# Performance work log

Hardware: AMD Instinct MI355X
Metric: run time of the kernel (lower is better)

## Reference

```python
import jax, jax.numpy as jnp
import numpy as np
from jax import lax

B, N, D, E, P, K, H = 32, 512, 512, 8, 96, 25, 4
PAD = 12  # conv padding so length is preserved


def setup_inputs() -> dict:
    key = jax.random.key(0)
    ks = jax.random.split(key, 16)
    s = 0.05  # weight scale to keep softmax/cosine well-conditioned
    x = jax.random.normal(ks[0], (B, N, D), dtype=jnp.float32)
    router = jax.random.normal(ks[1], (1, E, D), dtype=jnp.float32)
    Wq = jax.random.normal(ks[2], (D, D), dtype=jnp.float32) * s
    bq = jax.random.normal(ks[3], (D,), dtype=jnp.float32) * s
    Wk = jax.random.normal(ks[4], (D, D), dtype=jnp.float32) * s
    bk = jax.random.normal(ks[5], (D,), dtype=jnp.float32) * s
    Wv = jax.random.normal(ks[6], (D, D), dtype=jnp.float32) * s
    bv = jax.random.normal(ks[7], (D,), dtype=jnp.float32) * s
    Wo = jax.random.normal(ks[8], (D, D), dtype=jnp.float32) * s
    bo = jax.random.normal(ks[9], (D,), dtype=jnp.float32) * s
    Wc = jax.random.normal(ks[10], (E, 2, K), dtype=jnp.float32) * s  # E experts' Conv1d(2,1,25) stacked as out-channels
    bc = jax.random.normal(ks[11], (E,), dtype=jnp.float32) * s
    Wp = jax.random.normal(ks[12], (E, D, P), dtype=jnp.float32) * s  # E experts' Linear(D,P), stored (in,out)
    bp = jax.random.normal(ks[13], (E, P), dtype=jnp.float32) * s
    return {"x": x, "router": router, "Wq": Wq, "bq": bq, "Wk": Wk, "bk": bk,
            "Wv": Wv, "bv": bv, "Wo": Wo, "bo": bo, "Wc": Wc, "bc": bc,
            "Wp": Wp, "bp": bp}


def _forward(x, router, Wq, bq, Wk, bk, Wv, bv, Wo, bo, Wc, bc, Wp, bp):
    b, n, d = x.shape
    e = router.shape[1]
    dk = d // H
    r = jnp.broadcast_to(router, (b, e, d))
    # multi-head attention: queries=router slots, keys/values=x (dropout = identity at eval)
    q = (r @ Wq + bq).reshape(b, e, H, dk)
    k = (x @ Wk + bk).reshape(b, n, H, dk)
    v = (x @ Wv + bv).reshape(b, n, H, dk)
    scale = 1.0 / jnp.sqrt(jnp.asarray(dk, x.dtype))
    scores = jnp.einsum('blhe,bshe->bhls', q, k)  # [b,H,e,n]
    A = jax.nn.softmax(scale * scores, axis=-1)
    att = jnp.einsum('bhls,bshd->blhd', A, v).reshape(b, e, d)
    att = att @ Wo + bo  # [b,e,d]
    # cosine-similarity routing score, mapped to (1+pi)/2
    dot = jnp.einsum('bed,bnd->ben', att, x)
    norm_a = jnp.linalg.norm(att, axis=2, keepdims=True)          # [b,e,1]
    norm_x = jnp.linalg.norm(x, axis=2)[:, None, :]                # [b,1,n]
    score = (1.0 + dot / (norm_a * norm_x)) / 2.0                  # [b,e,n]
    idx = jnp.argmax(score, axis=1)                                # [b,n] expert per token
    z = jnp.take_along_axis(att, idx[:, :, None], axis=1)          # [b,n,d]
    result = jnp.stack([x, z], axis=-2).reshape(b * n, 2, d)       # [bn,2,d]
    # run all E expert convs at once (experts stacked as output channels)
    conv_out = lax.conv_general_dilated(
        result, Wc, window_strides=(1,), padding=[(PAD, PAD)],
        dimension_numbers=('NCH', 'OIH', 'NCH')) + bc[None, :, None]  # [bn,E,d]
    lin = jnp.einsum('nel,elp->nep', conv_out, Wp) + bp[None]         # [bn,E,P]
    flat_idx = idx.reshape(-1)
    out = jnp.take_along_axis(lin, flat_idx[:, None, None], axis=1)[:, 0, :]
    return out.reshape(b, n, P)


def reference(x, router, Wq, bq, Wk, bk, Wv, bv, Wo, bo, Wc, bc, Wp, bp):
    return _forward(x, router, Wq, bq, Wk, bk, Wv, bv, Wo, bo, Wc, bc, Wp, bp)
```

## Files before the change

kernel.cpp:

```cpp
#include <hip/hip_runtime.h>
#include <hip/hip_bf16.h>

#define B_ 32
#define N_ 512
#define D_ 512
#define E_ 8
#define P_ 96
#define KC 25
#define H_ 4
#define DK 128
#define HE 32
#define BN 16384

typedef short short8 __attribute__((ext_vector_type(8)));
typedef float f32x4 __attribute__((ext_vector_type(4)));

#define OCNT  4096
#define OS2   4352
#define OM    5120
#define OC    21504
#define OA    21536
#define OATT  676896
#define OTOK  807968
#define OWEFF 939040
#define OZC   1332256
#define OUP   1356832

__device__ __forceinline__ float b2f(short s) {
  unsigned u = ((unsigned)(unsigned short)s) << 16;
  return __builtin_bit_cast(float, u);
}
__device__ __forceinline__ unsigned short f2b(float f) {
  return __builtin_bit_cast(unsigned short, __float2bfloat16(f));
}

__global__ __launch_bounds__(256) void k_head(const float* __restrict__ router,
        const float* __restrict__ Wq, const float* __restrict__ bq,
        const float* __restrict__ Wk, const float* __restrict__ bk,
        const float* __restrict__ Wp, const float* __restrict__ Wc,
        float* __restrict__ M, float* __restrict__ c,
        int* __restrict__ cnt, float* __restrict__ s2,
        __hip_bfloat16* __restrict__ weff) {
  __shared__ float sm[5824];
  int bid = blockIdx.x;
  int tid = threadIdx.x;
  if (bid < 64) {
    float* rs = sm;
    float* ps = sm + 512;
    float* qs = sm + 768;
    int he = bid >> 1, ch = bid & 1;
    int h = he >> 3, e = he & 7;
    for (int i = tid; i < 512; i += 256) rs[i] = router[e * D_ + i];
    __syncthreads();
    {
      int j = tid & 127, dh = tid >> 7;
      const float* wq = Wq + h * 128 + j;
      float acc = 0.f;
      for (int d = dh * 256; d < dh * 256 + 256; d += 4) {
        acc = fmaf(rs[d], wq[d * D_], acc);
        acc = fmaf(rs[d + 1], wq[(d + 1) * D_], acc);
        acc = fmaf(rs[d + 2], wq[(d + 2) * D_], acc);
        acc = fmaf(rs[d + 3], wq[(d + 3) * D_], acc);
      }
      ps[dh * 128 + j] = acc;
    }
    __syncthreads();
    if (tid < 128) qs[tid] = ps[tid] + ps[128 + tid] + bq[h * 128 + tid];
    __syncthreads();
    {
      int d0 = ch * 256 + tid;
      const float* wrow = Wk + d0 * D_ + h * 128;
      float acc = 0.f;
      for (int jj = 0; jj < 128; jj += 4) {
        float4 wv = *(const float4*)(wrow + jj);
        acc = fmaf(wv.x, qs[jj], acc);
        acc = fmaf(wv.y, qs[jj + 1], acc);
        acc = fmaf(wv.z, qs[jj + 2], acc);
        acc = fmaf(wv.w, qs[jj + 3], acc);
      }
      M[he * D_ + d0] = acc;
    }
    if (ch == 0 && tid < 64) {
      float s = qs[tid] * bk[h * 128 + tid] + qs[tid + 64] * bk[h * 128 + tid + 64];
#pragma unroll
      for (int off = 32; off; off >>= 1) s += __shfl_xor(s, off);
      if (tid == 0) c[he] = s;
    }
  } else if (bid < 192) {
    float* T = sm;
    float* wcs = sm + 5760;
    int eb = bid - 64;
    int e = eb >> 4, mc = eb & 15;
    int lo = mc * 32 - 12;
    for (int idx = tid; idx < 56 * 24; idx += 256) {
      int lp = idx / 24, p4 = (idx - lp * 24) * 4;
      int l = lo + lp;
      float4 v = {0.f, 0.f, 0.f, 0.f};
      if (l >= 0 && l < D_) v = *(const float4*)(Wp + (e * D_ + l) * P_ + p4);
      T[p4 * 60 + lp] = v.x; T[(p4 + 1) * 60 + lp] = v.y;
      T[(p4 + 2) * 60 + lp] = v.z; T[(p4 + 3) * 60 + lp] = v.w;
    }
    if (tid < 50) wcs[tid] = Wc[e * 2 * KC + tid];
    __syncthreads();
    int m = tid & 31, pg = tid >> 5;
#pragma unroll
    for (int j = 0; j < 2; ++j)
      for (int k2 = 0; k2 < 12; ++k2) {
        int p = pg * 12 + k2;
        float acc = 0.f;
#pragma unroll
        for (int k = 0; k < KC; ++k)
          acc = fmaf(wcs[j * 25 + k], T[p * 60 + m - k + 24], acc);
        weff[(((e * 2 + j) * P_ + p) << 9) + mc * 32 + m] = __float2bfloat16(acc);
      }
  } else {
    int e = bid - 192;
    if (bid == 192) cnt[tid] = 0;
    if (tid < 192) {
      int p = tid % 96, lg = tid / 96;
      float s = 0.f;
      const float* wp = Wp + e * D_ * P_ + p;
      for (int l = lg * 256; l < lg * 256 + 256; ++l) s += wp[l * P_];
      sm[lg * 96 + p] = s;
    }
    __syncthreads();
    if (tid < 96) s2[e * 96 + tid] = sm[tid] + sm[96 + tid];
  }
}

__global__ __launch_bounds__(128) void k_logits(const float* __restrict__ x,
        const float* __restrict__ M, float* __restrict__ A0,
        float* __restrict__ A1) {
  __shared__ float xs[64 * 132];
  __shared__ float Ms[32 * 132];
  int dh = blockIdx.x & 1;
  int nt8 = (blockIdx.x >> 1) & 7;
  int b = blockIdx.x >> 4;
  int tid = threadIdx.x;
  const float* xb = x + (b * N_ + nt8 * 64) * D_ + dh * 256;
  const float* Mb = M + dh * 256;
  float acc[4][4] = {{0.f}};
  for (int kc = 0; kc < 2; ++kc) {
    for (int idx = tid; idx < 2048; idx += 128) {
      int r = idx >> 5, c4 = (idx & 31) * 4;
      *(float4*)(xs + r * 132 + c4) = *(const float4*)(xb + r * D_ + kc * 128 + c4);
    }
    for (int idx = tid; idx < 1024; idx += 128) {
      int r = idx >> 5, c4 = (idx & 31) * 4;
      *(float4*)(Ms + r * 132 + c4) = *(const float4*)(Mb + r * D_ + kc * 128 + c4);
    }
    __syncthreads();
    int nt = tid & 15, ht = tid >> 4;
#pragma unroll 4
    for (int d4 = 0; d4 < 128; d4 += 4) {
      float4 xv[4], mv[4];
#pragma unroll
      for (int i = 0; i < 4; ++i)
        xv[i] = *(const float4*)(xs + (nt + 16 * i) * 132 + d4);
#pragma unroll
      for (int j = 0; j < 4; ++j)
        mv[j] = *(const float4*)(Ms + (ht + 8 * j) * 132 + d4);
#pragma unroll
      for (int i = 0; i < 4; ++i)
#pragma unroll
        for (int j = 0; j < 4; ++j) {
          float s = acc[i][j];
          s = fmaf(xv[i].x, mv[j].x, s);
          s = fmaf(xv[i].y, mv[j].y, s);
          s = fmaf(xv[i].z, mv[j].z, s);
          s = fmaf(xv[i].w, mv[j].w, s);
          acc[i][j] = s;
        }
    }
    __syncthreads();
  }
  int nt = tid & 15, ht = tid >> 4;
  float* Ad = dh ? A1 : A0;
#pragma unroll
  for (int j = 0; j < 4; ++j) {
    int he = ht + 8 * j;
#pragma unroll
    for (int i = 0; i < 4; ++i)
      Ad[(b * HE + he) * N_ + nt8 * 64 + nt + 16 * i] = acc[i][j];
  }
}

__global__ __launch_bounds__(256) void k_softmax(float* __restrict__ A0,
        const float* __restrict__ A1, const float* __restrict__ c) {
  int row = blockIdx.x;
  float* p0 = A0 + row * N_;
  const float* p1 = A1 + row * N_;
  float cc = c[row & 31];
  int t = threadIdx.x;
  const float scale = 0.08838834764831845f;
  float v0 = scale * (p0[t] + p1[t] + cc);
  float v1 = scale * (p0[t + 256] + p1[t + 256] + cc);
  __shared__ float red[4], red2[4];
  float m = fmaxf(v0, v1);
#pragma unroll
  for (int off = 32; off; off >>= 1) m = fmaxf(m, __shfl_xor(m, off));
  if ((t & 63) == 0) red[t >> 6] = m;
  __syncthreads();
  m = fmaxf(fmaxf(red[0], red[1]), fmaxf(red[2], red[3]));
  float e0 = expf(v0 - m), e1 = expf(v1 - m);
  float s = e0 + e1;
#pragma unroll
  for (int off = 32; off; off >>= 1) s += __shfl_xor(s, off);
  if ((t & 63) == 0) red2[t >> 6] = s;
  __syncthreads();
  s = red2[0] + red2[1] + red2[2] + red2[3];
  float inv = 1.0f / s;
  p0[t] = e0 * inv;
  p0[t + 256] = e1 * inv;
}

__global__ __launch_bounds__(512) void k_u2(const float* __restrict__ x,
        const float* __restrict__ A, float* __restrict__ up) {
  __shared__ float As[64 * 33];
  int nq = blockIdx.x, b = blockIdx.y;
  for (int idx = threadIdx.x; idx < 64 * 32; idx += 512) {
    int n = idx & 63, he = idx >> 6;
    As[n * 33 + he] = A[(b * HE + he) * N_ + nq * 64 + n];
  }
  __syncthreads();
  int dq = threadIdx.x & 127, hg = threadIdx.x >> 7;
  const float* xb = x + (b * N_ + nq * 64) * D_ + dq * 4;
  float acc[8][4];
#pragma unroll
  for (int j = 0; j < 8; ++j)
#pragma unroll
    for (int k = 0; k < 4; ++k) acc[j][k] = 0.f;
  for (int n = 0; n < 64; ++n) {
    float4 xv = *(const float4*)(xb + n * D_);
    const float* ar = As + n * 33 + hg * 8;
#pragma unroll
    for (int j = 0; j < 8; ++j) {
      float a = ar[j];
      acc[j][0] = fmaf(a, xv.x, acc[j][0]);
      acc[j][1] = fmaf(a, xv.y, acc[j][1]);
      acc[j][2] = fmaf(a, xv.z, acc[j][2]);
      acc[j][3] = fmaf(a, xv.w, acc[j][3]);
    }
  }
  float* o = up + (((b * 8 + nq) * HE) + hg * 8) * D_ + dq * 4;
#pragma unroll
  for (int j = 0; j < 8; ++j) {
    float4 v; v.x = acc[j][0]; v.y = acc[j][1]; v.z = acc[j][2]; v.w = acc[j][3];
    *(float4*)(o + j * D_) = v;
  }
}

__global__ __launch_bounds__(512) void k_vo3(const float* __restrict__ up,
        const float* __restrict__ Wv, const float* __restrict__ bv,
        const float* __restrict__ Wo, const float* __restrict__ bo,
        float* __restrict__ att) {
  __shared__ float us[4 * 512];
  __shared__ float part[4 * 512];
  __shared__ float ap_s[512];
  int b = blockIdx.x >> 3, e = blockIdx.x & 7;
  int tid = threadIdx.x;
  for (int idx = tid; idx < 4 * 128; idx += 512) {
    int h = idx >> 7, d4 = (idx & 127) * 4;
    const float* base = up + ((b * 8) * HE + h * 8 + e) * D_ + d4;
    float4 s = {0.f, 0.f, 0.f, 0.f};
#pragma unroll
    for (int nq = 0; nq < 8; ++nq) {
      float4 v = *(const float4*)(base + nq * HE * D_);
      s.x += v.x; s.y += v.y; s.z += v.z; s.w += v.w;
    }
    *(float4*)(us + h * 512 + d4) = s;
  }
  __syncthreads();
  {
    int cch = tid >> 7, j = tid & 127;
    int i0 = j * 4;
    int h = j >> 5;
    const float* ur = us + h * 512;
    const float* wv = Wv + i0;
    float4 acc = {0.f, 0.f, 0.f, 0.f};
    int d0 = cch * 128;
#pragma unroll 4
    for (int d = d0; d < d0 + 128; ++d) {
      float4 wq = *(const float4*)(wv + d * D_);
      float a = ur[d];
      acc.x = fmaf(a, wq.x, acc.x);
      acc.y = fmaf(a, wq.y, acc.y);
      acc.z = fmaf(a, wq.z, acc.z);
      acc.w = fmaf(a, wq.w, acc.w);
    }
    *(float4*)(part + cch * 512 + i0) = acc;
  }
  __syncthreads();
  ap_s[tid] = part[tid] + part[512 + tid] + part[1024 + tid] + part[1536 + tid]
              + bv[tid];
  __syncthreads();
  {
    int cch = tid >> 7, j = tid & 127;
    int o0 = j * 4;
    const float* wo = Wo + o0;
    float4 acc = {0.f, 0.f, 0.f, 0.f};
    int i0 = cch * 128;
#pragma unroll 4
    for (int i = i0; i < i0 + 128; ++i) {
      float4 wq = *(const float4*)(wo + i * D_);
      float a = ap_s[i];
      acc.x = fmaf(a, wq.x, acc.x);
      acc.y = fmaf(a, wq.y, acc.y);
      acc.z = fmaf(a, wq.z, acc.z);
      acc.w = fmaf(a, wq.w, acc.w);
    }
    *(float4*)(part + cch * 512 + o0) = acc;
  }
  __syncthreads();
  att[(b * E_ + e) * D_ + tid] = part[tid] + part[512 + tid] + part[1024 + tid]
                                 + part[1536 + tid] + bo[tid];
}

__global__ __launch_bounds__(256) void k_route2(const float* __restrict__ x,
        const float* __restrict__ att, const __hip_bfloat16* __restrict__ weff,
        const float* __restrict__ s2, const float* __restrict__ bc,
        const float* __restrict__ bp, int* __restrict__ cnt,
        int* __restrict__ tok, float* __restrict__ zc) {
  __shared__ float att_s[8 * D_];
  __shared__ float rn[8];
  __shared__ float red[4][520];
  __shared__ int blist[8][32];
  __shared__ int bcnt[8];
  int b = blockIdx.x >> 4, tile = blockIdx.x & 15;
  for (int idx = threadIdx.x; idx < 1024; idx += 256)
    *(float4*)(att_s + idx * 4) = *(const float4*)(att + b * E_ * D_ + idx * 4);
  if (threadIdx.x < 8) bcnt[threadIdx.x] = 0;
  __syncthreads();
  {
    int e = threadIdx.x >> 5, l = threadIdx.x & 31;
    float s = 0.f;
    for (int d0 = l; d0 < D_; d0 += 32) {
      float v = att_s[e * D_ + d0];
      s = fmaf(v, v, s);
    }
#pragma unroll
    for (int off = 16; off; off >>= 1) s += __shfl_xor(s, off);
    if (l == 0) rn[e] = 1.0f / sqrtf(s);
  }
  __syncthreads();
  int w = threadIdx.x >> 6, lane = threadIdx.x & 63;
  int e2 = lane & 7, ch = lane >> 3;
  float* rw = red[w];
  for (int i = 0; i < 8; ++i) {
    int t = b * N_ + tile * 32 + w * 8 + i;
    const float* xp = x + t * D_ + lane * 8;
    float4 xa = *(const float4*)xp;
    float4 xb4 = *(const float4*)(xp + 4);
    float p[8];
#pragma unroll
    for (int e = 0; e < 8; ++e) {
      const float* apt = att_s + e * D_ + lane * 8;
      float4 a0 = *(const float4*)apt;
      float4 a1 = *(const float4*)(apt + 4);
      float s = a0.x * xa.x;
      s = fmaf(a0.y, xa.y, s); s = fmaf(a0.z, xa.z, s); s = fmaf(a0.w, xa.w, s);
      s = fmaf(a1.x, xb4.x, s); s = fmaf(a1.y, xb4.y, s);
      s = fmaf(a1.z, xb4.z, s); s = fmaf(a1.w, xb4.w, s);
      p[e] = s;
    }
#pragma unroll
    for (int e = 0; e < 8; ++e) rw[e * 65 + lane] = p[e];
    float s = 0.f;
#pragma unroll
    for (int k = 0; k < 8; ++k) s += rw[e2 * 65 + ch * 8 + k];
    s += __shfl_xor(s, 8); s += __shfl_xor(s, 16); s += __shfl_xor(s, 32);
    float sc = s * rn[e2];
    int be = e2;
#pragma unroll
    for (int off = 1; off < 8; off <<= 1) {
      float o = __shfl_xor(sc, off);
      int oe = __shfl_xor(be, off);
      if (o > sc || (o == sc && oe < be)) { sc = o; be = oe; }
    }
    if (lane == 0) {
      int slot = atomicAdd(&bcnt[be], 1);
      blist[be][slot] = t;
    }
  }
  __syncthreads();
  {
    int e = threadIdx.x >> 5, r = threadIdx.x & 31;
    int ce = bcnt[e];
    int gs = 0;
    if (r == 0 && ce > 0) gs = atomicAdd(&cnt[e * 32], ce);
    gs = __shfl(gs, (threadIdx.x & 63) & 32);
    for (int k2 = r; k2 < ce; k2 += 32) tok[e * BN + gs + k2] = blist[e][k2];
  }
  int grp = threadIdx.x >> 4, l16 = threadIdx.x & 15;
  for (int r = 0; r < 3; ++r) {
    int P = tile * 48 + r * 16 + grp;
    int ez = P / 96, p = P - ez * 96;
    const short* wrow = (const short*)weff + (((ez * 2 + 1) * P_ + p) << 9);
    const float* arow = att_s + ez * D_;
    float acc = 0.f;
#pragma unroll
    for (int seg = 0; seg < 4; ++seg) {
      int d = seg * 128 + l16 * 8;
      short8 w8 = *(const short8*)(wrow + d);
      const float* a8 = arow + d;
      acc = fmaf(a8[0], b2f(w8[0]), acc); acc = fmaf(a8[1], b2f(w8[1]), acc);
      acc = fmaf(a8[2], b2f(w8[2]), acc); acc = fmaf(a8[3], b2f(w8[3]), acc);
      acc = fmaf(a8[4], b2f(w8[4]), acc); acc = fmaf(a8[5], b2f(w8[5]), acc);
      acc = fmaf(a8[6], b2f(w8[6]), acc); acc = fmaf(a8[7], b2f(w8[7]), acc);
    }
    acc += __shfl_xor(acc, 1); acc += __shfl_xor(acc, 2);
    acc += __shfl_xor(acc, 4); acc += __shfl_xor(acc, 8);
    if (l16 == 0)
      zc[(b * E_ + ez) * P_ + p] = acc + bc[ez] * s2[ez * 96 + p] + bp[ez * 96 + p];
  }
}

__global__ __launch_bounds__(256) void k_final(const float* __restrict__ x,
        const __hip_bfloat16* __restrict__ weff, const float* __restrict__ zc,
        const int* __restrict__ cnt, const int* __restrict__ tok,
        float* __restrict__ out) {
  __shared__ __align__(16) unsigned short xsb[32 * 520];
  __shared__ int toks[32];
  int g = blockIdx.x;
  int cl_e[E_], bs[E_ + 1];
  bs[0] = 0;
#pragma unroll
  for (int e = 0; e < E_; ++e) {
    cl_e[e] = cnt[e * 32];
    bs[e + 1] = bs[e] + ((cl_e[e] + 31) >> 5);
  }
  if (g >= bs[E_]) return;
  int e = 0;
#pragma unroll
  for (int k = 1; k < E_; ++k) if (g >= bs[k]) e = k;
  int base = (g - bs[e]) * 32;
  int cnt_e = cl_e[e];
  int cl = cnt_e - base; if (cl > 32) cl = 32;
  int tid = threadIdx.x;
  if (tid < 32) toks[tid] = (tid < cl) ? tok[e * BN + base + tid] : tok[e * BN + base];
  __syncthreads();
  for (int idx = tid; idx < 32 * 128; idx += 256) {
    int r = idx >> 7, c4 = (idx & 127) * 4;
    float4 v = *(const float4*)(x + toks[r] * D_ + c4);
    ushort4 u4;
    u4.x = f2b(v.x); u4.y = f2b(v.y); u4.z = f2b(v.z); u4.w = f2b(v.w);
    *(ushort4*)(xsb + r * 520 + c4) = u4;
  }
  __syncthreads();
  int wave = tid >> 6, lane = tid & 63;
  int mw = wave & 1, nw = wave >> 1;
  int m16 = lane & 15, quad = lane >> 4;
  const short* w0 = (const short*)(weff + (e * 2 + 0) * P_ * D_);
  f32x4 acc[3];
#pragma unroll
  for (int nt = 0; nt < 3; ++nt) acc[nt] = (f32x4){0.f, 0.f, 0.f, 0.f};
  const short* arow = (const short*)xsb + (mw * 16 + m16) * 520 + quad * 8;
  const short* brow = w0 + (nw * 48 + m16) * D_ + quad * 8;
  for (int kt = 0; kt < 16; ++kt) {
    int koff = kt * 32;
    short8 a = *(const short8*)(arow + koff);
#pragma unroll
    for (int nt = 0; nt < 3; ++nt) {
      short8 bf = *(const short8*)(brow + nt * 16 * D_ + koff);
      acc[nt] = __builtin_amdgcn_mfma_f32_16x16x32_bf16(a, bf, acc[nt], 0, 0, 0);
    }
  }
#pragma unroll
  for (int nt = 0; nt < 3; ++nt)
#pragma unroll
    for (int rr = 0; rr < 4; ++rr) {
      int row = mw * 16 + quad * 4 + rr;
      if (row < cl) {
        int tg = toks[row];
        int bb = tg >> 9;
        int p = nw * 48 + nt * 16 + m16;
        out[tg * P_ + p] = acc[nt][rr] + zc[(bb * E_ + e) * P_ + p];
      }
    }
}

extern "C" void kernel_launch(void* const* d_in, const int* in_sizes, int n_in,
                              void* d_out, int out_size, void* d_ws, size_t ws_size,
                              hipStream_t stream) {
  const float* x      = (const float*)d_in[0];
  const float* router = (const float*)d_in[1];
  const float* Wq     = (const float*)d_in[2];
  const float* bq     = (const float*)d_in[3];
  const float* Wk     = (const float*)d_in[4];
  const float* bk     = (const float*)d_in[5];
  const float* Wv     = (const float*)d_in[6];
  const float* bv     = (const float*)d_in[7];
  const float* Wo     = (const float*)d_in[8];
  const float* bo     = (const float*)d_in[9];
  const float* Wc     = (const float*)d_in[10];
  const float* bc     = (const float*)d_in[11];
  const float* Wp     = (const float*)d_in[12];
  const float* bp     = (const float*)d_in[13];
  float* out = (float*)d_out;
  float* w = (float*)d_ws;

  int*   cnt  = (int*)(w + OCNT);
  float* s2   = w + OS2;
  float* M    = w + OM;
  float* c    = w + OC;
  float* A0   = w + OA;
  float* A1   = w + OUP;
  float* att  = w + OATT;
  int*   tok  = (int*)(w + OTOK);
  __hip_bfloat16* weff = (__hip_bfloat16*)(w + OWEFF);
  float* zc   = w + OZC;
  float* up   = w + OUP;

  k_head<<<200, 256, 0, stream>>>(router, Wq, bq, Wk, bk, Wp, Wc, M, c, cnt, s2, weff);
  k_logits<<<512, 128, 0, stream>>>(x, M, A0, A1);
  k_softmax<<<1024, 256, 0, stream>>>(A0, A1, c);
  k_u2<<<dim3(8, 32), 512, 0, stream>>>(x, A0, up);
  k_vo3<<<256, 512, 0, stream>>>(up, Wv, bv, Wo, bo, att);
  k_route2<<<512, 256, 0, stream>>>(x, att, weff, s2, bc, bp, cnt, tok, zc);
  k_final<<<520, 256, 0, stream>>>(x, weff, zc, cnt, tok, out);
}
```

Baseline: 226.7 us.

## Fuse softmax into attention-weighted sum kernel, recomputing row stats per block

Removes the separate softmax kernel. Each block of the attention-value accumulation kernel now recomputes the per-row max and sum over all 32 head-slot rows of its batch, then normalizes its 64-column slice while staging it into shared memory. A1 moves to its own workspace region because the output buffer can no longer alias it. This saves a kernel launch and one write and reread of the probability matrix, at the cost of each of the 8 blocks per batch redundantly reading full logit rows.

```diff
diff --git a/kernel.cpp b/kernel.cpp
--- a/kernel.cpp
+++ b/kernel.cpp
@@ -25,6 +25,7 @@
 #define OWEFF 939040
 #define OZC   1332256
 #define OUP   1356832
+#define OA1   5551136
 
 __device__ __forceinline__ float b2f(short s) {
   unsigned u = ((unsigned)(unsigned short)s) << 16;
@@ -185,45 +186,49 @@
   }
 }
 
-__global__ __launch_bounds__(256) void k_softmax(float* __restrict__ A0,
-        const float* __restrict__ A1, const float* __restrict__ c) {
-  int row = blockIdx.x;
-  float* p0 = A0 + row * N_;
-  const float* p1 = A1 + row * N_;
-  float cc = c[row & 31];
-  int t = threadIdx.x;
+__global__ __launch_bounds__(512) void k_u3(const float* __restrict__ x,
+        const float* __restrict__ A0, const float* __restrict__ A1,
+        const float* __restrict__ c, float* __restrict__ up) {
+  __shared__ float As[64 * 33];
+  __shared__ float mS[32], sS[32];
+  int nq = blockIdx.x, b = blockIdx.y;
+  int tid = threadIdx.x;
   const float scale = 0.08838834764831845f;
-  float v0 = scale * (p0[t] + p1[t] + cc);
-  float v1 = scale * (p0[t + 256] + p1[t + 256] + cc);
-  __shared__ float red[4], red2[4];
-  float m = fmaxf(v0, v1);
-#pragma unroll
-  for (int off = 32; off; off >>= 1) m = fmaxf(m, __shfl_xor(m, off));
-  if ((t & 63) == 0) red[t >> 6] = m;
-  __syncthreads();
-  m = fmaxf(fmaxf(red[0], red[1]), fmaxf(red[2], red[3]));
-  float e0 = expf(v0 - m), e1 = expf(v1 - m);
-  float s = e0 + e1;
-#pragma unroll
-  for (int off = 32; off; off >>= 1) s += __shfl_xor(s, off);
-  if ((t & 63) == 0) red2[t >> 6] = s;
-  __syncthreads();
-  s = red2[0] + red2[1] + red2[2] + red2[3];
-  float inv = 1.0f / s;
-  p0[t] = e0 * inv;
-  p0[t + 256] = e1 * inv;
-}
-
-__global__ __launch_bounds__(512) void k_u2(const float* __restrict__ x,
-        const float* __restrict__ A, float* __restrict__ up) {
-  __shared__ float As[64 * 33];
-  int nq = blockIdx.x, b = blockIdx.y;
-  for (int idx = threadIdx.x; idx < 64 * 32; idx += 512) {
+  {
+    int wv = tid >> 6, lane = tid & 63;
+    int he = wv * 4 + (lane >> 4);
+    int l16 = lane & 15;
+    const float* r0 = A0 + (b * HE + he) * N_;
+    const float* r1 = A1 + (b * HE + he) * N_;
+    float cc = c[he];
+    float v[32];
+    float m = -1e30f;
+#pragma unroll
+    for (int k = 0; k < 32; ++k) {
+      int n = l16 + k * 16;
+      float vv = scale * (r0[n] + r1[n] + cc);
+      v[k] = vv;
+      m = fmaxf(m, vv);
+    }
+    m = fmaxf(m, __shfl_xor(m, 1)); m = fmaxf(m, __shfl_xor(m, 2));
+    m = fmaxf(m, __shfl_xor(m, 4)); m = fmaxf(m, __shfl_xor(m, 8));
+    float s = 0.f;
+#pragma unroll
+    for (int k = 0; k < 32; ++k) s += expf(v[k] - m);
+    s += __shfl_xor(s, 1); s += __shfl_xor(s, 2);
+    s += __shfl_xor(s, 4); s += __shfl_xor(s, 8);
+    if (l16 == 0) { mS[he] = m; sS[he] = 1.0f / s; }
+  }
+  __syncthreads();
+  for (int idx = tid; idx < 64 * 32; idx += 512) {
     int n = idx & 63, he = idx >> 6;
-    As[n * 33 + he] = A[(b * HE + he) * N_ + nq * 64 + n];
-  }
-  __syncthreads();
-  int dq = threadIdx.x & 127, hg = threadIdx.x >> 7;
+    int gn = nq * 64 + n;
+    float vv = scale * (A0[(b * HE + he) * N_ + gn] + A1[(b * HE + he) * N_ + gn]
+                        + c[he]);
+    As[n * 33 + he] = expf(vv - mS[he]) * sS[he];
+  }
+  __syncthreads();
+  int dq = tid & 127, hg = tid >> 7;
   const float* xb = x + (b * N_ + nq * 64) * D_ + dq * 4;
   float acc[8][4];
 #pragma unroll
@@ -504,7 +509,7 @@
   float* M    = w + OM;
   float* c    = w + OC;
   float* A0   = w + OA;
-  float* A1   = w + OUP;
+  float* A1   = w + OA1;
   float* att  = w + OATT;
   int*   tok  = (int*)(w + OTOK);
   __hip_bfloat16* weff = (__hip_bfloat16*)(w + OWEFF);
@@ -513,8 +518,7 @@
 
   k_head<<<200, 256, 0, stream>>>(router, Wq, bq, Wk, bk, Wp, Wc, M, c, cnt, s2, weff);
   k_logits<<<512, 128, 0, stream>>>(x, M, A0, A1);
-  k_softmax<<<1024, 256, 0, stream>>>(A0, A1, c);
-  k_u2<<<dim3(8, 32), 512, 0, stream>>>(x, A0, up);
+  k_u3<<<dim3(8, 32), 512, 0, stream>>>(x, A0, A1, c, up);
   k_vo3<<<256, 512, 0, stream>>>(up, Wv, bv, Wo, bo, att);
   k_route2<<<512, 256, 0, stream>>>(x, att, weff, s2, bc, bp, cnt, tok, zc);
   k_final<<<520, 256, 0, stream>>>(x, weff, zc, cnt, tok, out);
```

Result: no change. 222.4 us (-1.9%).
